# Optimization experiments

Hardware: AMD Instinct MI355X
Metric: run time of the kernel (lower is better)

Reference implementation:

```python
import jax, jax.numpy as jnp
import numpy as np

BETA = 0.9
THRESH = 1.0
SLOPE = 25.0  # snntorch fast_sigmoid default slope
T = 4096

@jax.custom_vjp
def spike_fn(x):
    # Heaviside forward, fast-sigmoid surrogate backward
    return (x > 0).astype(x.dtype)

def _spike_fwd(x):
    return (x > 0).astype(x.dtype), x

def _spike_bwd(x, g):
    return (g / (SLOPE * jnp.abs(x) + 1.0) ** 2,)

spike_fn.defvjp(_spike_fwd, _spike_bwd)

def setup_inputs():
    key = jax.random.key(0)
    ks = jax.random.split(key, 5)
    B = 1024
    x = jax.random.normal(ks[0], (B, 6, T), dtype=jnp.float32)
    W1 = jax.random.normal(ks[1], (10, 6), dtype=jnp.float32) / np.sqrt(6.0)
    b1 = jax.random.normal(ks[2], (10,), dtype=jnp.float32) * 0.01
    W2 = jax.random.normal(ks[3], (27, 10), dtype=jnp.float32) / np.sqrt(10.0)
    b2 = jax.random.normal(ks[4], (27,), dtype=jnp.float32) * 0.01
    return {"x": x, "W1": W1, "b1": b1, "W2": W2, "b2": b2}

def reference(x, W1, b1, W2, b2):
    B = x.shape[0]
    xt = jnp.transpose(x, (2, 0, 1))  # [T, B, 6]
    mem1_0 = jnp.zeros((B, 10), x.dtype)
    mem2_0 = jnp.zeros((B, 27), x.dtype)

    def step(carry, xin):
        mem1, mem2 = carry
        cur1 = xin @ W1.T + b1                              # [B,10]
        rst1 = jax.lax.stop_gradient((mem1 > THRESH).astype(x.dtype))
        mem1 = BETA * mem1 + cur1 - rst1 * THRESH           # subtract reset
        spk1 = spike_fn(mem1 - THRESH)
        cur2 = spk1 @ W2.T + b2                             # [B,27]
        rst2 = jax.lax.stop_gradient((mem2 > THRESH).astype(x.dtype))
        mem2 = BETA * mem2 + cur2 - rst2 * THRESH
        return (mem1, mem2), None

    (mem1, mem2), _ = jax.lax.scan(step, (mem1_0, mem2_0), xt)
    # module returns only the spike of the final timestep
    return spike_fn(mem2 - THRESH)
```

## Files before the change

kernel.cpp:

```cpp
#include <hip/hip_runtime.h>


#define T_STEPS 4096
#define BETA 0.9f
#define THRESH 1.0f
#define CH 64
#define NCHUNK (T_STEPS / CH)
#define GRP 8
#define NGRP (CH / GRP)

__global__ __launch_bounds__(128, 1) void snn_kernel(
    const float* __restrict__ x,
    const float* __restrict__ W1,
    const float* __restrict__ b1,
    const float* __restrict__ W2,
    const float* __restrict__ b2,
    float* __restrict__ out)
{
    __shared__ float tabLo[32 * 32];
    __shared__ float tabHi[32 * 32];
    __shared__ float curBuf[10 * 68];
    __shared__ unsigned maskBuf[2][64];

    const int tid = threadIdx.x;
    const int wid = tid >> 6;
    const int l   = tid & 63;
    const int b   = blockIdx.x;

    if (tid < 32) {
        for (int j = 0; j < 27; ++j) {
            float slo = b2[j];
            float shi = 0.0f;
            #pragma unroll
            for (int i = 0; i < 5; ++i) {
                if (tid & (1 << i)) {
                    slo += W2[j * 10 + i];
                    shi += W2[j * 10 + 5 + i];
                }
            }
            tabLo[tid * 32 + j] = slo;
            tabHi[tid * 32 + j] = shi;
        }
    }

    float w1r[60], b1r[10];
    float xv[6], xn[6];
    float mem1 = 0.0f;
    bool  sp1 = false;
    const int ri = (l < 10) ? l : 9;
    const float* cp = &curBuf[ri * 68];
    const float* xb = x + (size_t)b * 6 * T_STEPS;

    if (wid == 0) {
        #pragma unroll
        for (int i = 0; i < 10; ++i) {
            b1r[i] = b1[i];
            #pragma unroll
            for (int c = 0; c < 6; ++c) w1r[i * 6 + c] = W1[i * 6 + c];
        }
        #pragma unroll
        for (int c = 0; c < 6; ++c) xv[c] = xb[c * T_STEPS + l];
    }

    float mem2 = 0.0f;
    bool  sp2 = false;
    const int rj = (l < 27) ? l : 26;

    __syncthreads();

    #pragma unroll 1
    for (int k = 0; k <= NCHUNK; ++k) {
        if (wid == 0 && k < NCHUNK) {
            #pragma unroll
            for (int i = 0; i < 10; ++i) {
                float acc = xv[0] * w1r[i * 6 + 0];
                acc = fmaf(xv[1], w1r[i * 6 + 1], acc);
                acc = fmaf(xv[2], w1r[i * 6 + 2], acc);
                acc = fmaf(xv[3], w1r[i * 6 + 3], acc);
                acc = fmaf(xv[4], w1r[i * 6 + 4], acc);
                acc = fmaf(xv[5], w1r[i * 6 + 5], acc);
                curBuf[i * 68 + l] = acc + b1r[i];
            }
            if (k + 1 < NCHUNK) {
                #pragma unroll
                for (int c = 0; c < 6; ++c) xn[c] = xb[c * T_STEPS + (k + 1) * CH + l];
            }

            unsigned vmask = 0u;
            float c1v[8];
            {
                float4 q0 = *(const float4*)(cp + 0);
                float4 q1 = *(const float4*)(cp + 4);
                c1v[0] = q0.x; c1v[1] = q0.y; c1v[2] = q0.z; c1v[3] = q0.w;
                c1v[4] = q1.x; c1v[5] = q1.y; c1v[6] = q1.z; c1v[7] = q1.w;
            }
            #pragma unroll
            for (int g = 0; g < NGRP; ++g) {
                float c1n[8];
                if (g + 1 < NGRP) {
                    float4 p0 = *(const float4*)(cp + (g + 1) * 8);
                    float4 p1 = *(const float4*)(cp + (g + 1) * 8 + 4);
                    c1n[0] = p0.x; c1n[1] = p0.y; c1n[2] = p0.z; c1n[3] = p0.w;
                    c1n[4] = p1.x; c1n[5] = p1.y; c1n[6] = p1.z; c1n[7] = p1.w;
                }
                #pragma unroll
                for (int s = 0; s < 8; ++s) {
                    float t1 = fmaf(BETA, mem1, c1v[s]);
                    mem1 = sp1 ? (t1 - THRESH) : t1;
                    sp1 = mem1 > THRESH;
                    unsigned m = (unsigned)__ballot(sp1);
                    vmask = (l == g * 8 + s) ? m : vmask;
                }
                if (g + 1 < NGRP) {
                    #pragma unroll
                    for (int s = 0; s < 8; ++s) c1v[s] = c1n[s];
                }
            }
            maskBuf[k & 1][l] = vmask;
        }

        if (wid == 1 && k >= 1) {
            unsigned vmask = maskBuf[(k - 1) & 1][l];

            unsigned mlo[GRP], mhi[GRP];
            float tlo[GRP], thi[GRP];
            #pragma unroll
            for (int s = 0; s < 8; ++s) {
                unsigned m = (unsigned)__builtin_amdgcn_readlane((int)vmask, s);
                mlo[s] = (m & 31u) << 5;
                mhi[s] = ((m >> 5) & 31u) << 5;
            }
            #pragma unroll
            for (int s = 0; s < 8; ++s) {
                tlo[s] = tabLo[mlo[s] + rj];
                thi[s] = tabHi[mhi[s] + rj];
            }

            #pragma unroll
            for (int g = 0; g < NGRP; ++g) {
                unsigned nlo[GRP], nhi[GRP];
                float ntl[GRP], nth[GRP];
                if (g + 1 < NGRP) {
                    #pragma unroll
                    for (int s = 0; s < 8; ++s) {
                        unsigned m = (unsigned)__builtin_amdgcn_readlane(
                            (int)vmask, (g + 1) * 8 + s);
                        nlo[s] = (m & 31u) << 5;
                        nhi[s] = ((m >> 5) & 31u) << 5;
                    }
                    #pragma unroll
                    for (int s = 0; s < 8; ++s) {
                        ntl[s] = tabLo[nlo[s] + rj];
                        nth[s] = tabHi[nhi[s] + rj];
                    }
                }
                #pragma unroll
                for (int s = 0; s < 8; ++s) {
                    float cur2 = tlo[s] + thi[s];
                    float t2 = fmaf(BETA, mem2, cur2);
                    mem2 = sp2 ? (t2 - THRESH) : t2;
                    sp2 = mem2 > THRESH;
                }
                if (g + 1 < NGRP) {
                    #pragma unroll
                    for (int s = 0; s < 8; ++s) { tlo[s] = ntl[s]; thi[s] = nth[s]; }
                }
            }
        }

        if (wid == 0 && k + 1 < NCHUNK) {
            #pragma unroll
            for (int c = 0; c < 6; ++c) xv[c] = xn[c];
        }

        __syncthreads();
    }

    if (wid == 1 && l < 27) {
        out[b * 27 + l] = sp2 ? 1.0f : 0.0f;
    }
}

extern "C" void kernel_launch(void* const* d_in, const int* in_sizes, int n_in,
                              void* d_out, int out_size, void* d_ws, size_t ws_size,
                              hipStream_t stream) {
    const float* x  = (const float*)d_in[0];
    const float* W1 = (const float*)d_in[1];
    const float* b1 = (const float*)d_in[2];
    const float* W2 = (const float*)d_in[3];
    const float* b2 = (const float*)d_in[4];
    float* out = (float*)d_out;

    const int B = in_sizes[0] / (6 * T_STEPS);
    snn_kernel<<<dim3(B), dim3(128), 0, stream>>>(x, W1, b1, W2, b2, out);
}
```

Baseline: 312.7 us.

## Split layer-2 into a three-stage wave pipeline with a cur2 table-lookup wave

Adds a third wavefront so that one wave computes layer-1 spikes, a second turns the spike masks into cur2 values through the precomputed table lookups and writes them to a double-buffered shared array, and a third runs the layer-2 membrane recurrence from plain float4 loads. The aim is to take the readlane and table-gather latency off the serial layer-2 recurrence. In exchange the block grows to 192 threads, the pipeline gets one more chunk of fill latency, and more shared memory is used.

```diff
diff --git a/kernel.cpp b/kernel.cpp
--- a/kernel.cpp
+++ b/kernel.cpp
@@ -9,7 +9,7 @@
 #define GRP 8
 #define NGRP (CH / GRP)
 
-__global__ __launch_bounds__(128, 1) void snn_kernel(
+__global__ __launch_bounds__(192, 1) void snn_kernel(
     const float* __restrict__ x,
     const float* __restrict__ W1,
     const float* __restrict__ b1,
@@ -21,6 +21,7 @@
     __shared__ float tabHi[32 * 32];
     __shared__ float curBuf[10 * 68];
     __shared__ unsigned maskBuf[2][64];
+    __shared__ float cur2Buf[2][27 * 68];
 
     const int tid = threadIdx.x;
     const int wid = tid >> 6;
@@ -62,6 +63,10 @@
         for (int c = 0; c < 6; ++c) xv[c] = xb[c * T_STEPS + l];
     }
 
+    const int gh = l >> 5;
+    const int gjr = l & 31;
+    const int gj = (gjr < 27) ? gjr : 26;
+
     float mem2 = 0.0f;
     bool  sp2 = false;
     const int rj = (l < 27) ? l : 26;
@@ -69,7 +74,7 @@
     __syncthreads();
 
     #pragma unroll 1
-    for (int k = 0; k <= NCHUNK; ++k) {
+    for (int k = 0; k <= NCHUNK + 1; ++k) {
         if (wid == 0 && k < NCHUNK) {
             #pragma unroll
             for (int i = 0; i < 10; ++i) {
@@ -117,66 +122,64 @@
                 }
             }
             maskBuf[k & 1][l] = vmask;
+
+            if (k + 1 < NCHUNK) {
+                #pragma unroll
+                for (int c = 0; c < 6; ++c) xv[c] = xn[c];
+            }
         }
 
-        if (wid == 1 && k >= 1) {
-            unsigned vmask = maskBuf[(k - 1) & 1][l];
+        if (wid == 1 && k >= 1 && k <= NCHUNK) {
+            const int par = (k - 1) & 1;
+            const unsigned* mrow = &maskBuf[par][gh];
+            float* crow = &cur2Buf[par][gj * 68 + gh];
 
-            unsigned mlo[GRP], mhi[GRP];
-            float tlo[GRP], thi[GRP];
+            unsigned mr[32];
             #pragma unroll
-            for (int s = 0; s < 8; ++s) {
-                unsigned m = (unsigned)__builtin_amdgcn_readlane((int)vmask, s);
-                mlo[s] = (m & 31u) << 5;
-                mhi[s] = ((m >> 5) & 31u) << 5;
+            for (int r = 0; r < 32; ++r) mr[r] = mrow[2 * r];
+            #pragma unroll
+            for (int r = 0; r < 32; ++r) {
+                unsigned alo = (mr[r] & 31u) << 5;
+                unsigned ahi = ((mr[r] >> 5) & 31u) << 5;
+                crow[2 * r] = tabLo[alo + gj] + tabHi[ahi + gj];
+            }
+        }
+
+        if (wid == 2 && k >= 2) {
+            const float* cp2 = &cur2Buf[(k - 2) & 1][rj * 68];
+            float c2v[8];
+            {
+                float4 q0 = *(const float4*)(cp2 + 0);
+                float4 q1 = *(const float4*)(cp2 + 4);
+                c2v[0] = q0.x; c2v[1] = q0.y; c2v[2] = q0.z; c2v[3] = q0.w;
+                c2v[4] = q1.x; c2v[5] = q1.y; c2v[6] = q1.z; c2v[7] = q1.w;
             }
             #pragma unroll
-            for (int s = 0; s < 8; ++s) {
-                tlo[s] = tabLo[mlo[s] + rj];
-                thi[s] = tabHi[mhi[s] + rj];
-            }
-
-            #pragma unroll
             for (int g = 0; g < NGRP; ++g) {
-                unsigned nlo[GRP], nhi[GRP];
-                float ntl[GRP], nth[GRP];
+                float c2n[8];
                 if (g + 1 < NGRP) {
-                    #pragma unroll
-                    for (int s = 0; s < 8; ++s) {
-                        unsigned m = (unsigned)__builtin_amdgcn_readlane(
-                            (int)vmask, (g + 1) * 8 + s);
-                        nlo[s] = (m & 31u) << 5;
-                        nhi[s] = ((m >> 5) & 31u) << 5;
-                    }
-                    #pragma unroll
-                    for (int s = 0; s < 8; ++s) {
-                        ntl[s] = tabLo[nlo[s] + rj];
-                        nth[s] = tabHi[nhi[s] + rj];
-                    }
+                    float4 p0 = *(const float4*)(cp2 + (g + 1) * 8);
+                    float4 p1 = *(const float4*)(cp2 + (g + 1) * 8 + 4);
+                    c2n[0] = p0.x; c2n[1] = p0.y; c2n[2] = p0.z; c2n[3] = p0.w;
+                    c2n[4] = p1.x; c2n[5] = p1.y; c2n[6] = p1.z; c2n[7] = p1.w;
                 }
                 #pragma unroll
                 for (int s = 0; s < 8; ++s) {
-                    float cur2 = tlo[s] + thi[s];
-                    float t2 = fmaf(BETA, mem2, cur2);
+                    float t2 = fmaf(BETA, mem2, c2v[s]);
                     mem2 = sp2 ? (t2 - THRESH) : t2;
                     sp2 = mem2 > THRESH;
                 }
                 if (g + 1 < NGRP) {
                     #pragma unroll
-                    for (int s = 0; s < 8; ++s) { tlo[s] = ntl[s]; thi[s] = nth[s]; }
+                    for (int s = 0; s < 8; ++s) c2v[s] = c2n[s];
                 }
             }
-        }
-
-        if (wid == 0 && k + 1 < NCHUNK) {
-            #pragma unroll
-            for (int c = 0; c < 6; ++c) xv[c] = xn[c];
         }
 
         __syncthreads();
     }
 
-    if (wid == 1 && l < 27) {
+    if (wid == 2 && l < 27) {
         out[b * 27 + l] = sp2 ? 1.0f : 0.0f;
     }
 }
@@ -192,5 +195,5 @@
     float* out = (float*)d_out;
 
     const int B = in_sizes[0] / (6 * T_STEPS);
-    snn_kernel<<<dim3(B), dim3(128), 0, stream>>>(x, W1, b1, W2, b2, out);
+    snn_kernel<<<dim3(B), dim3(192), 0, stream>>>(x, W1, b1, W2, b2, out);
 }
```

Measured after the change: 302.3 us. 3.3% less time.

## Pack two batch elements per block using wavefront halves

Applied to the files above, without the earlier changes.

Each block now handles two batch elements. Each 64-lane wavefront is split into two 32-lane halves, one per element, so the grid shrinks to B/2 blocks. The layer-1 ballot is compacted into a 20-bit mask holding both elements' spikes, and the layer-2 wave reads the masks from shared memory with vector loads instead of using readlane. The goal is better use of lanes that sat idle in the serial recurrences (only 10 and 27 lanes were active). The cost is twice the layer-1 current computation per wave, and each block now runs a single long serial chain per wave for two elements.

```diff
diff --git a/kernel.cpp b/kernel.cpp
--- a/kernel.cpp
+++ b/kernel.cpp
@@ -19,13 +19,16 @@
 {
     __shared__ float tabLo[32 * 32];
     __shared__ float tabHi[32 * 32];
-    __shared__ float curBuf[10 * 68];
+    __shared__ float curBuf[20 * 68];
     __shared__ unsigned maskBuf[2][64];
 
     const int tid = threadIdx.x;
     const int wid = tid >> 6;
     const int l   = tid & 63;
+    const int h   = l >> 5;
+    const int li  = l & 31;
     const int b   = blockIdx.x;
+    const int e   = 2 * b + h;
 
     if (tid < 32) {
         for (int j = 0; j < 27; ++j) {
@@ -44,12 +47,12 @@
     }
 
     float w1r[60], b1r[10];
-    float xv[6], xn[6];
+    float xv[2][6], xn[2][6];
     float mem1 = 0.0f;
     bool  sp1 = false;
-    const int ri = (l < 10) ? l : 9;
-    const float* cp = &curBuf[ri * 68];
-    const float* xb = x + (size_t)b * 6 * T_STEPS;
+    const int ri = (li < 10) ? li : 9;
+    const float* cp = &curBuf[(h * 10 + ri) * 68];
+    const float* xb = x + (size_t)e * 6 * T_STEPS;
 
     if (wid == 0) {
         #pragma unroll
@@ -59,12 +62,16 @@
             for (int c = 0; c < 6; ++c) w1r[i * 6 + c] = W1[i * 6 + c];
         }
         #pragma unroll
-        for (int c = 0; c < 6; ++c) xv[c] = xb[c * T_STEPS + l];
+        for (int p = 0; p < 2; ++p)
+            #pragma unroll
+            for (int c = 0; c < 6; ++c) xv[p][c] = xb[c * T_STEPS + p * 32 + li];
     }
 
     float mem2 = 0.0f;
     bool  sp2 = false;
-    const int rj = (l < 27) ? l : 26;
+    const int jc = (li < 27) ? li : 26;
+    const int ofsLo = h * 10;
+    const int ofsHi = h * 10 + 5;
 
     __syncthreads();
 
@@ -72,18 +79,24 @@
     for (int k = 0; k <= NCHUNK; ++k) {
         if (wid == 0 && k < NCHUNK) {
             #pragma unroll
-            for (int i = 0; i < 10; ++i) {
-                float acc = xv[0] * w1r[i * 6 + 0];
-                acc = fmaf(xv[1], w1r[i * 6 + 1], acc);
-                acc = fmaf(xv[2], w1r[i * 6 + 2], acc);
-                acc = fmaf(xv[3], w1r[i * 6 + 3], acc);
-                acc = fmaf(xv[4], w1r[i * 6 + 4], acc);
-                acc = fmaf(xv[5], w1r[i * 6 + 5], acc);
-                curBuf[i * 68 + l] = acc + b1r[i];
+            for (int p = 0; p < 2; ++p) {
+                #pragma unroll
+                for (int i = 0; i < 10; ++i) {
+                    float acc = xv[p][0] * w1r[i * 6 + 0];
+                    acc = fmaf(xv[p][1], w1r[i * 6 + 1], acc);
+                    acc = fmaf(xv[p][2], w1r[i * 6 + 2], acc);
+                    acc = fmaf(xv[p][3], w1r[i * 6 + 3], acc);
+                    acc = fmaf(xv[p][4], w1r[i * 6 + 4], acc);
+                    acc = fmaf(xv[p][5], w1r[i * 6 + 5], acc);
+                    curBuf[(h * 10 + i) * 68 + p * 32 + li] = acc + b1r[i];
+                }
             }
             if (k + 1 < NCHUNK) {
                 #pragma unroll
-                for (int c = 0; c < 6; ++c) xn[c] = xb[c * T_STEPS + (k + 1) * CH + l];
+                for (int p = 0; p < 2; ++p)
+                    #pragma unroll
+                    for (int c = 0; c < 6; ++c)
+                        xn[p][c] = xb[c * T_STEPS + (k + 1) * CH + p * 32 + li];
             }
 
             unsigned vmask = 0u;
@@ -108,8 +121,10 @@
                     float t1 = fmaf(BETA, mem1, c1v[s]);
                     mem1 = sp1 ? (t1 - THRESH) : t1;
                     sp1 = mem1 > THRESH;
-                    unsigned m = (unsigned)__ballot(sp1);
-                    vmask = (l == g * 8 + s) ? m : vmask;
+                    unsigned long long bal = __ballot(sp1);
+                    unsigned mC = (unsigned)((bal & 0x3FFull) |
+                                             ((bal >> 22) & 0xFFC00ull));
+                    vmask = (l == g * 8 + s) ? mC : vmask;
                 }
                 if (g + 1 < NGRP) {
                     #pragma unroll
@@ -117,41 +132,44 @@
                 }
             }
             maskBuf[k & 1][l] = vmask;
+
+            if (k + 1 < NCHUNK) {
+                #pragma unroll
+                for (int p = 0; p < 2; ++p)
+                    #pragma unroll
+                    for (int c = 0; c < 6; ++c) xv[p][c] = xn[p][c];
+            }
         }
 
         if (wid == 1 && k >= 1) {
-            unsigned vmask = maskBuf[(k - 1) & 1][l];
-
-            unsigned mlo[GRP], mhi[GRP];
-            float tlo[GRP], thi[GRP];
-            #pragma unroll
-            for (int s = 0; s < 8; ++s) {
-                unsigned m = (unsigned)__builtin_amdgcn_readlane((int)vmask, s);
-                mlo[s] = (m & 31u) << 5;
-                mhi[s] = ((m >> 5) & 31u) << 5;
-            }
-            #pragma unroll
-            for (int s = 0; s < 8; ++s) {
-                tlo[s] = tabLo[mlo[s] + rj];
-                thi[s] = tabHi[mhi[s] + rj];
-            }
-
+            const unsigned* mrow = maskBuf[(k - 1) & 1];
+
+            float tlo[8], thi[8];
+            {
+                uint4 m0 = *(const uint4*)(mrow + 0);
+                uint4 m1 = *(const uint4*)(mrow + 4);
+                unsigned mv[8] = {m0.x, m0.y, m0.z, m0.w, m1.x, m1.y, m1.z, m1.w};
+                #pragma unroll
+                for (int s = 0; s < 8; ++s) {
+                    unsigned rl = (mv[s] >> ofsLo) & 31u;
+                    unsigned rh = (mv[s] >> ofsHi) & 31u;
+                    tlo[s] = tabLo[rl * 32 + jc];
+                    thi[s] = tabHi[rh * 32 + jc];
+                }
+            }
             #pragma unroll
             for (int g = 0; g < NGRP; ++g) {
-                unsigned nlo[GRP], nhi[GRP];
-                float ntl[GRP], nth[GRP];
-                if (g + 1 < NGRP) {
+                float ntl[8], nth[8];
+                if (g + 1 < NGRP) {
+                    uint4 m0 = *(const uint4*)(mrow + (g + 1) * 8);
+                    uint4 m1 = *(const uint4*)(mrow + (g + 1) * 8 + 4);
+                    unsigned mv[8] = {m0.x, m0.y, m0.z, m0.w, m1.x, m1.y, m1.z, m1.w};
                     #pragma unroll
                     for (int s = 0; s < 8; ++s) {
-                        unsigned m = (unsigned)__builtin_amdgcn_readlane(
-                            (int)vmask, (g + 1) * 8 + s);
-                        nlo[s] = (m & 31u) << 5;
-                        nhi[s] = ((m >> 5) & 31u) << 5;
-                    }
-                    #pragma unroll
-                    for (int s = 0; s < 8; ++s) {
-                        ntl[s] = tabLo[nlo[s] + rj];
-                        nth[s] = tabHi[nhi[s] + rj];
+                        unsigned rl = (mv[s] >> ofsLo) & 31u;
+                        unsigned rh = (mv[s] >> ofsHi) & 31u;
+                        ntl[s] = tabLo[rl * 32 + jc];
+                        nth[s] = tabHi[rh * 32 + jc];
                     }
                 }
                 #pragma unroll
@@ -168,16 +186,11 @@
             }
         }
 
-        if (wid == 0 && k + 1 < NCHUNK) {
-            #pragma unroll
-            for (int c = 0; c < 6; ++c) xv[c] = xn[c];
-        }
-
         __syncthreads();
     }
 
-    if (wid == 1 && l < 27) {
-        out[b * 27 + l] = sp2 ? 1.0f : 0.0f;
+    if (wid == 1 && li < 27) {
+        out[e * 27 + li] = sp2 ? 1.0f : 0.0f;
     }
 }
 
@@ -192,5 +205,5 @@
     float* out = (float*)d_out;
 
     const int B = in_sizes[0] / (6 * T_STEPS);
-    snn_kernel<<<dim3(B), dim3(128), 0, stream>>>(x, W1, b1, W2, b2, out);
+    snn_kernel<<<dim3(B / 2), dim3(128), 0, stream>>>(x, W1, b1, W2, b2, out);
 }
```

Result: slower. 335.3 us (+7.2%).
